# Kernel tuning notes

Measured on AMD Instinct MI355X. Metric: run time of the kernel, lower is better.

The kernel has to match this reference:

```python
import jax, jax.numpy as jnp
import numpy as np

EPS = 1e-8
TEMPERATURE = 1.0


def setup_inputs() -> dict:
    key = jax.random.key(0)
    k1, k2, k3 = jax.random.split(key, 3)
    B, Q, K, H, D = 64, 64, 8192, 1, 64
    return {
        "query": jax.random.normal(k1, (B, Q, H, D), dtype=jnp.float32),
        "key": jax.random.normal(k2, (B, K, H, D), dtype=jnp.float32),
        "value": jax.random.normal(k3, (B, K, H, D), dtype=jnp.float32),
    }


def reference(query, key, value):
    # InvertedDotProductAttention(norm_type='mean', multi_head=False)
    d = query.shape[-1]
    q = query / jnp.sqrt(jnp.asarray(d, query.dtype))
    # logits: [B, H, Q, K]
    attn = jnp.einsum("bqhd,bkhd->bhqk", q, key)
    # inverted attention: softmax over the QUERY axis (-2)
    attn = jax.nn.softmax(attn / TEMPERATURE, axis=-2)
    attn = jnp.clip(attn, 0.0, 1.0)
    # renormalize over keys (norm_type == 'mean')
    attn = attn / (jnp.sum(attn, axis=-1, keepdims=True) + EPS)
    out = jnp.einsum("bhqk,bkhd->bqhd", attn, value)
    # single-head: squeeze heads dim
    out = jnp.squeeze(out, axis=-2)          # [B, Q, Dv]
    attn_weights = jnp.squeeze(attn, axis=-3)  # [B, Q, K]
    return out, attn_weights
```

## Files before the change

### kernel.cpp

```cpp
#include <hip/hip_runtime.h>
#include <cstddef>

#define NB 64
#define NQ 64
#define NK 8192
#define ND 64
#define KPB 256
#define KSL 512
#define NSLICE (NK / KSL)

typedef __attribute__((ext_vector_type(8))) short short8_t;
typedef __attribute__((ext_vector_type(8))) unsigned short ushort8_t;
typedef __attribute__((ext_vector_type(4))) unsigned short ushort4_t;
typedef __attribute__((ext_vector_type(4))) float float4_t;

static __device__ __forceinline__ unsigned short f2bf(float f) {
    unsigned b = __float_as_uint(f);
    b += 0x7FFFu + ((b >> 16) & 1u);
    return (unsigned short)(b >> 16);
}
static __device__ __forceinline__ float bf2f(unsigned short u) {
    return __uint_as_float(((unsigned)u) << 16);
}
static __device__ __forceinline__ void split8(const float* f, short8_t& hi, short8_t& lo) {
#pragma unroll
    for (int j = 0; j < 8; ++j) {
        const unsigned u = __float_as_uint(f[j]);
        hi[j] = (short)(u >> 16);
        const float lof = f[j] - __uint_as_float(u & 0xFFFF0000u);
        lo[j] = (short)(__float_as_uint(lof) >> 16);
    }
}

__global__ __launch_bounds__(256, 3) void k_qk_p(
    const float* __restrict__ query,
    const float* __restrict__ key,
    unsigned short* __restrict__ pstore,
    float* __restrict__ rowsum)
{
    __shared__ alignas(16) unsigned short SH[64 * 264];
    unsigned short* Qhi = SH;
    unsigned short* Qlo = SH + 64 * 72;

    const int tid  = threadIdx.x;
    const int b    = blockIdx.y;
    const int k0   = blockIdx.x * KPB;
    const int lane = tid & 63;
    const int w    = tid >> 6;
    const int lq   = lane & 15;
    const int lg   = lane >> 4;

    float kf[16];
    {
        const float* kr = key + ((size_t)b * NK + k0 + w * 64 + lq) * ND + lg * 8;
        *reinterpret_cast<float4*>(kf)      = *reinterpret_cast<const float4*>(kr);
        *reinterpret_cast<float4*>(kf + 4)  = *reinterpret_cast<const float4*>(kr + 4);
        *reinterpret_cast<float4*>(kf + 8)  = *reinterpret_cast<const float4*>(kr + 32);
        *reinterpret_cast<float4*>(kf + 12) = *reinterpret_cast<const float4*>(kr + 36);
    }

    {
        const float* qb = query + (size_t)b * NQ * ND;
#pragma unroll
        for (int i = 0; i < 2; ++i) {
            const int o  = tid + 256 * i;
            const int q  = o >> 3;
            const int d0 = (o & 7) * 8;
            float f[8];
            *reinterpret_cast<float4*>(f)     = *reinterpret_cast<const float4*>(qb + q * ND + d0);
            *reinterpret_cast<float4*>(f + 4) = *reinterpret_cast<const float4*>(qb + q * ND + d0 + 4);
            short8_t h, l8;
            split8(f, h, l8);
            const int n    = q >> 4;
            const int l    = (q & 15) | (((d0 >> 3) & 3) << 4);
            const int dh   = d0 >> 5;
            const int base = l * 72 + n * 16 + dh * 8;
            *reinterpret_cast<short8_t*>(&Qhi[base]) = h;
            *reinterpret_cast<short8_t*>(&Qlo[base]) = l8;
        }
    }
    __syncthreads();

    short8_t bhi[4][2], blo[4][2];
#pragma unroll
    for (int n = 0; n < 4; ++n)
#pragma unroll
        for (int dh = 0; dh < 2; ++dh) {
            const int base = lane * 72 + n * 16 + dh * 8;
            bhi[n][dh] = *reinterpret_cast<const short8_t*>(&Qhi[base]);
            blo[n][dh] = *reinterpret_cast<const short8_t*>(&Qlo[base]);
        }
    __syncthreads();

    unsigned short* pL = SH;
    float rsacc[4] = {0.f, 0.f, 0.f, 0.f};

#pragma unroll 1
    for (int s = 0; s < 4; ++s) {
        const int kbase = k0 + w * 64 + s * 16;

        short8_t ahi[2], alo[2];
        split8(kf, ahi[0], alo[0]);
        split8(kf + 8, ahi[1], alo[1]);

        if (s < 3) {
            const float* kr = key + ((size_t)b * NK + kbase + 16 + lq) * ND + lg * 8;
            *reinterpret_cast<float4*>(kf)      = *reinterpret_cast<const float4*>(kr);
            *reinterpret_cast<float4*>(kf + 4)  = *reinterpret_cast<const float4*>(kr + 4);
            *reinterpret_cast<float4*>(kf + 8)  = *reinterpret_cast<const float4*>(kr + 32);
            *reinterpret_cast<float4*>(kf + 12) = *reinterpret_cast<const float4*>(kr + 36);
        }

        float4_t acc[4];
#pragma unroll
        for (int n = 0; n < 4; ++n) acc[n] = (float4_t){0.f, 0.f, 0.f, 0.f};
#pragma unroll
        for (int n = 0; n < 4; ++n)
#pragma unroll
            for (int dh = 0; dh < 2; ++dh) {
                acc[n] = __builtin_amdgcn_mfma_f32_16x16x32_bf16(ahi[dh], bhi[n][dh], acc[n], 0, 0, 0);
                acc[n] = __builtin_amdgcn_mfma_f32_16x16x32_bf16(ahi[dh], blo[n][dh], acc[n], 0, 0, 0);
                acc[n] = __builtin_amdgcn_mfma_f32_16x16x32_bf16(alo[dh], bhi[n][dh], acc[n], 0, 0, 0);
            }

        float m[4], z[4];
#pragma unroll
        for (int r = 0; r < 4; ++r) {
            m[r] = fmaxf(fmaxf(acc[0][r], acc[1][r]), fmaxf(acc[2][r], acc[3][r]));
            m[r] = fmaxf(m[r], __shfl_xor(m[r], 1, 64));
            m[r] = fmaxf(m[r], __shfl_xor(m[r], 2, 64));
            m[r] = fmaxf(m[r], __shfl_xor(m[r], 4, 64));
            m[r] = fmaxf(m[r], __shfl_xor(m[r], 8, 64));
            z[r] = 0.f;
        }
#pragma unroll
        for (int n = 0; n < 4; ++n)
#pragma unroll
            for (int r = 0; r < 4; ++r) {
                acc[n][r] = __expf((acc[n][r] - m[r]) * 0.125f);
                z[r] += acc[n][r];
            }
#pragma unroll
        for (int r = 0; r < 4; ++r) {
            z[r] += __shfl_xor(z[r], 1, 64);
            z[r] += __shfl_xor(z[r], 2, 64);
            z[r] += __shfl_xor(z[r], 4, 64);
            z[r] += __shfl_xor(z[r], 8, 64);
            z[r] = 1.f / z[r];
        }

#pragma unroll
        for (int n = 0; n < 4; ++n) {
            ushort4_t u;
            float rs = 0.f;
#pragma unroll
            for (int r = 0; r < 4; ++r) {
                u[r] = f2bf(acc[n][r] * z[r]);
                rs += bf2f(u[r]);
            }
            *reinterpret_cast<ushort4_t*>(
                &pL[(16 * n + lq) * 264 + w * 64 + s * 16 + lg * 4]) = u;
            rs += __shfl_xor(rs, 16, 64);
            rs += __shfl_xor(rs, 32, 64);
            rsacc[n] += rs;
        }
    }

    if (lg == 0) {
#pragma unroll
        for (int n = 0; n < 4; ++n)
            atomicAdd(&rowsum[b * NQ + lq + 16 * n], rsacc[n]);
    }
    __syncthreads();

    {
        const int cl = tid & 63;
#pragma unroll
        for (int t = 0; t < 16; ++t) {
            const int row = t * 4 + w;
            const ushort4_t u = *reinterpret_cast<const ushort4_t*>(&pL[row * 264 + cl * 4]);
            const int c      = cl * 4;
            const int half   = c >> 7;
            const int slot   = (c & 127) >> 3;
            const int sub    = (c >> 2) & 1;
            const int sp     = slot ^ (row & 7);
            *reinterpret_cast<ushort4_t*>(pstore +
                ((size_t)(b * NQ + row)) * NK + k0 + half * 128 + sp * 8 + sub * 4) = u;
        }
    }
}

template<bool PART>
__global__ __launch_bounds__(256, 4) void k_scale_pv(
    const unsigned short* __restrict__ psrc,
    const float* __restrict__ value,
    const float* __restrict__ rowsum,
    float* __restrict__ attn,
    float* __restrict__ dst)
{
    __shared__ alignas(16) unsigned short pLu[64 * 128];
    __shared__ float rsL[NQ];

    const int tid  = threadIdx.x;
    const int b    = blockIdx.y;
    const int ks   = blockIdx.x;
    const int k0   = ks * KSL;
    const int lane = tid & 63;
    const int w    = tid >> 6;
    const int lq   = lane & 15;
    const int lg   = lane >> 4;

    if (tid < NQ) rsL[tid] = 1.f / (rowsum[b * NQ + tid] + 1e-8f);

    const unsigned short* pg = psrc + (size_t)b * NQ * NK;
    const float* vcol = value + ((size_t)b * NK + k0) * ND + 16 * w + lq;

    ushort8_t rp[4];
    float vfA[32], vfB[32];

#define LOADP(HT)                                                              \
    {                                                                          \
        _Pragma("unroll")                                                      \
        for (int i = 0; i < 4; ++i) {                                          \
            const int idx = tid + 256 * i;                                     \
            rp[i] = *reinterpret_cast<const ushort8_t*>(                       \
                &pg[(size_t)(idx >> 4) * NK + k0 + (HT) * 128 + (idx & 15) * 8]); \
        }                                                                      \
    }

#define LOADV(VF, HT)                                                          \
    {                                                                          \
        _Pragma("unroll")                                                      \
        for (int h = 0; h < 4; ++h) {                                          \
            _Pragma("unroll")                                                  \
            for (int j = 0; j < 8; ++j)                                        \
                VF[h * 8 + j] =                                                \
                    vcol[(size_t)((HT) * 128 + h * 32 + lg * 8 + j) * ND];     \
        }                                                                      \
    }

#define STAGE_P(HT)                                                            \
    {                                                                          \
        _Pragma("unroll")                                                      \
        for (int i = 0; i < 4; ++i) {                                          \
            const int idx  = tid + 256 * i;                                    \
            const int row  = idx >> 4;                                         \
            const int sl   = idx & 15;                                         \
            const int slog = sl ^ (row & 7);                                   \
            const float iv = rsL[row];                                         \
            float f[8];                                                        \
            ushort8_t u;                                                       \
            _Pragma("unroll")                                                  \
            for (int j = 0; j < 8; ++j) {                                      \
                f[j] = bf2f(rp[i][j]) * iv;                                    \
                u[j] = f2bf(f[j]);                                             \
            }                                                                  \
            float* ap = attn + ((size_t)(b * NQ + row)) * NK + k0 +            \
                        (HT) * 128 + slog * 8;                                 \
            *reinterpret_cast<float4*>(ap)     = *reinterpret_cast<float4*>(f);     \
            *reinterpret_cast<float4*>(ap + 4) = *reinterpret_cast<float4*>(f + 4); \
            *reinterpret_cast<ushort8_t*>(&pLu[idx * 8]) = u;                  \
        }                                                                      \
    }

#define PVSTEP(VF)                                                             \
    {                                                                          \
        _Pragma("unroll")                                                      \
        for (int h = 0; h < 4; ++h) {                                          \
            short8_t vb;                                                       \
            _Pragma("unroll")                                                  \
            for (int j = 0; j < 8; ++j) vb[j] = (short)f2bf(VF[h * 8 + j]);    \
            _Pragma("unroll")                                                  \
            for (int n = 0; n < 4; ++n) {                                      \
                const short8_t pa = *reinterpret_cast<const short8_t*>(        \
                    &pLu[(16 * n + lq) * 128 + (((h * 4 + lg) ^ (lq & 7)) * 8)]); \
                oacc[n] = __builtin_amdgcn_mfma_f32_16x16x32_bf16(pa, vb, oacc[n], 0, 0, 0); \
            }                                                                  \
        }                                                                      \
    }

    float4_t oacc[4];
#pragma unroll
    for (int n = 0; n < 4; ++n) oacc[n] = (float4_t){0.f, 0.f, 0.f, 0.f};

    LOADP(0); LOADV(vfA, 0);

    __syncthreads();
    STAGE_P(0);
    LOADP(1); LOADV(vfB, 1);
    __syncthreads();
    PVSTEP(vfA);
    __syncthreads();
    STAGE_P(1);
    LOADP(2); LOADV(vfA, 2);
    __syncthreads();
    PVSTEP(vfB);
    __syncthreads();
    STAGE_P(2);
    LOADP(3); LOADV(vfB, 3);
    __syncthreads();
    PVSTEP(vfA);
    __syncthreads();
    STAGE_P(3);
    __syncthreads();
    PVSTEP(vfB);

#undef LOADP
#undef LOADV
#undef STAGE_P
#undef PVSTEP

    if (PART) {
        float* pb = dst + ((size_t)(b * NSLICE + ks)) * (NQ * ND);
#pragma unroll
        for (int n = 0; n < 4; ++n)
#pragma unroll
            for (int r = 0; r < 4; ++r)
                pb[(16 * n + 4 * lg + r) * ND + 16 * w + lq] = oacc[n][r];
    } else {
#pragma unroll
        for (int n = 0; n < 4; ++n)
#pragma unroll
            for (int r = 0; r < 4; ++r)
                atomicAdd(dst + ((size_t)(b * NQ + 16 * n + 4 * lg + r)) * ND + 16 * w + lq,
                          oacc[n][r]);
    }
}

__global__ __launch_bounds__(256) void k_reduce_out(
    const float* __restrict__ partials,
    float* __restrict__ out)
{
    const int b   = blockIdx.y;
    const int idx = blockIdx.x * 256 + threadIdx.x;
    const float4* pb = reinterpret_cast<const float4*>(partials + (size_t)b * NSLICE * NQ * ND);
    float4 sum = make_float4(0.f, 0.f, 0.f, 0.f);
#pragma unroll
    for (int s = 0; s < NSLICE; ++s) {
        const float4 v = pb[(size_t)s * (NQ * ND / 4) + idx];
        sum.x += v.x; sum.y += v.y; sum.z += v.z; sum.w += v.w;
    }
    reinterpret_cast<float4*>(out + (size_t)b * NQ * ND)[idx] = sum;
}

extern "C" void kernel_launch(void* const* d_in, const int* in_sizes, int n_in,
                              void* d_out, int out_size, void* d_ws, size_t ws_size,
                              hipStream_t stream) {
    const float* query = (const float*)d_in[0];
    const float* key   = (const float*)d_in[1];
    const float* value = (const float*)d_in[2];

    float* out  = (float*)d_out;
    float* attn = (float*)d_out + (size_t)NB * NQ * ND;

    const size_t PB_BYTES   = (size_t)NB * NQ * NK * sizeof(unsigned short);
    const size_t PART_BYTES = (size_t)NB * NSLICE * NQ * ND * sizeof(float);

    float* rowsum = (float*)d_ws;
    unsigned short* pbuf = (unsigned short*)((char*)d_ws + 16384);
    float* partials = (float*)((char*)d_ws + 16384 + PB_BYTES);
    const bool part = ws_size >= 16384 + PB_BYTES + PART_BYTES;

    hipMemsetAsync(rowsum, 0, (size_t)NB * NQ * sizeof(float), stream);
    if (!part)
        hipMemsetAsync(out, 0, (size_t)NB * NQ * ND * sizeof(float), stream);

    dim3 gA(NK / KPB, NB);
    k_qk_p<<<gA, 256, 0, stream>>>(query, key, pbuf, rowsum);

    dim3 gB(NK / KSL, NB);
    if (part) {
        k_scale_pv<true><<<gB, 256, 0, stream>>>(pbuf, value, rowsum, attn, partials);
        k_reduce_out<<<dim3(4, NB), 256, 0, stream>>>(partials, out);
    } else {
        k_scale_pv<false><<<gB, 256, 0, stream>>>(pbuf, value, rowsum, attn, out);
    }
}
```

Before: 122.5 us.

## Fuse PV product into QK kernel and defer row normalization to output

Moves the P·V matmul into the QK/softmax kernel, using unnormalized P from shared memory and loading V per 256-key tile. The final row-sum normalization is applied afterwards, in the reduction or a separate scaling kernel. The attention-weight scaling becomes a standalone streaming kernel that reads bf16 P and writes fp32 attn. This removes a sync-heavy staging pipeline, at the cost of more registers in the fused kernel and a partial-sum buffer twice as large.

```diff
diff --git a/kernel.cpp b/kernel.cpp
--- a/kernel.cpp
+++ b/kernel.cpp
@@ -6,8 +6,7 @@
 #define NK 8192
 #define ND 64
 #define KPB 256
-#define KSL 512
-#define NSLICE (NK / KSL)
+#define NSLICE (NK / KPB)
 
 typedef __attribute__((ext_vector_type(8))) short short8_t;
 typedef __attribute__((ext_vector_type(8))) unsigned short ushort8_t;
@@ -32,11 +31,14 @@
     }
 }
 
-__global__ __launch_bounds__(256, 3) void k_qk_p(
+template<bool PART>
+__global__ __launch_bounds__(256, 3) void k_fused(
     const float* __restrict__ query,
     const float* __restrict__ key,
+    const float* __restrict__ value,
     unsigned short* __restrict__ pstore,
-    float* __restrict__ rowsum)
+    float* __restrict__ rowsum,
+    float* __restrict__ dst)
 {
     __shared__ alignas(16) unsigned short SH[64 * 264];
     unsigned short* Qhi = SH;
@@ -49,6 +51,19 @@
     const int w    = tid >> 6;
     const int lq   = lane & 15;
     const int lg   = lane >> 4;
+
+    const float* vcol = value + ((size_t)b * NK + k0) * ND + 16 * w + lq;
+    float vfA[16], vfB[16];
+#pragma unroll
+    for (int h = 0; h < 2; ++h)
+#pragma unroll
+        for (int j = 0; j < 8; ++j)
+            vfA[h * 8 + j] = vcol[(size_t)(h * 32 + lg * 8 + j) * ND];
+#pragma unroll
+    for (int h = 0; h < 2; ++h)
+#pragma unroll
+        for (int j = 0; j < 8; ++j)
+            vfB[h * 8 + j] = vcol[(size_t)(64 + h * 32 + lg * 8 + j) * ND];
 
     float kf[16];
     {
@@ -159,7 +174,7 @@
                 rs += bf2f(u[r]);
             }
             *reinterpret_cast<ushort4_t*>(
-                &pL[(16 * n + lq) * 264 + w * 64 + s * 16 + lg * 4]) = u;
+                &pL[(16 * n + lq) * 264 + (kbase - k0) + lg * 4]) = u;
             rs += __shfl_xor(rs, 16, 64);
             rs += __shfl_xor(rs, 32, 64);
             rsacc[n] += rs;
@@ -173,145 +188,45 @@
     }
     __syncthreads();
 
-    {
-        const int cl = tid & 63;
-#pragma unroll
-        for (int t = 0; t < 16; ++t) {
-            const int row = t * 4 + w;
-            const ushort4_t u = *reinterpret_cast<const ushort4_t*>(&pL[row * 264 + cl * 4]);
-            const int c      = cl * 4;
-            const int half   = c >> 7;
-            const int slot   = (c & 127) >> 3;
-            const int sub    = (c >> 2) & 1;
-            const int sp     = slot ^ (row & 7);
-            *reinterpret_cast<ushort4_t*>(pstore +
-                ((size_t)(b * NQ + row)) * NK + k0 + half * 128 + sp * 8 + sub * 4) = u;
-        }
-    }
-}
-
-template<bool PART>
-__global__ __launch_bounds__(256, 4) void k_scale_pv(
-    const unsigned short* __restrict__ psrc,
-    const float* __restrict__ value,
-    const float* __restrict__ rowsum,
-    float* __restrict__ attn,
-    float* __restrict__ dst)
-{
-    __shared__ alignas(16) unsigned short pLu[64 * 128];
-    __shared__ float rsL[NQ];
-
-    const int tid  = threadIdx.x;
-    const int b    = blockIdx.y;
-    const int ks   = blockIdx.x;
-    const int k0   = ks * KSL;
-    const int lane = tid & 63;
-    const int w    = tid >> 6;
-    const int lq   = lane & 15;
-    const int lg   = lane >> 4;
-
-    if (tid < NQ) rsL[tid] = 1.f / (rowsum[b * NQ + tid] + 1e-8f);
-
-    const unsigned short* pg = psrc + (size_t)b * NQ * NK;
-    const float* vcol = value + ((size_t)b * NK + k0) * ND + 16 * w + lq;
-
-    ushort8_t rp[4];
-    float vfA[32], vfB[32];
-
-#define LOADP(HT)                                                              \
+    float4_t oacc[4];
+#pragma unroll
+    for (int n = 0; n < 4; ++n) oacc[n] = (float4_t){0.f, 0.f, 0.f, 0.f};
+
+#define PVCHUNK(VF, C)                                                         \
     {                                                                          \
         _Pragma("unroll")                                                      \
-        for (int i = 0; i < 4; ++i) {                                          \
-            const int idx = tid + 256 * i;                                     \
-            rp[i] = *reinterpret_cast<const ushort8_t*>(                       \
-                &pg[(size_t)(idx >> 4) * NK + k0 + (HT) * 128 + (idx & 15) * 8]); \
-        }                                                                      \
-    }
-
-#define LOADV(VF, HT)                                                          \
-    {                                                                          \
-        _Pragma("unroll")                                                      \
-        for (int h = 0; h < 4; ++h) {                                          \
-            _Pragma("unroll")                                                  \
-            for (int j = 0; j < 8; ++j)                                        \
-                VF[h * 8 + j] =                                                \
-                    vcol[(size_t)((HT) * 128 + h * 32 + lg * 8 + j) * ND];     \
-        }                                                                      \
-    }
-
-#define STAGE_P(HT)                                                            \
-    {                                                                          \
-        _Pragma("unroll")                                                      \
-        for (int i = 0; i < 4; ++i) {                                          \
-            const int idx  = tid + 256 * i;                                    \
-            const int row  = idx >> 4;                                         \
-            const int sl   = idx & 15;                                         \
-            const int slog = sl ^ (row & 7);                                   \
-            const float iv = rsL[row];                                         \
-            float f[8];                                                        \
-            ushort8_t u;                                                       \
-            _Pragma("unroll")                                                  \
-            for (int j = 0; j < 8; ++j) {                                      \
-                f[j] = bf2f(rp[i][j]) * iv;                                    \
-                u[j] = f2bf(f[j]);                                             \
-            }                                                                  \
-            float* ap = attn + ((size_t)(b * NQ + row)) * NK + k0 +            \
-                        (HT) * 128 + slog * 8;                                 \
-            *reinterpret_cast<float4*>(ap)     = *reinterpret_cast<float4*>(f);     \
-            *reinterpret_cast<float4*>(ap + 4) = *reinterpret_cast<float4*>(f + 4); \
-            *reinterpret_cast<ushort8_t*>(&pLu[idx * 8]) = u;                  \
-        }                                                                      \
-    }
-
-#define PVSTEP(VF)                                                             \
-    {                                                                          \
-        _Pragma("unroll")                                                      \
-        for (int h = 0; h < 4; ++h) {                                          \
+        for (int h = 0; h < 2; ++h) {                                          \
             short8_t vb;                                                       \
             _Pragma("unroll")                                                  \
             for (int j = 0; j < 8; ++j) vb[j] = (short)f2bf(VF[h * 8 + j]);    \
             _Pragma("unroll")                                                  \
             for (int n = 0; n < 4; ++n) {                                      \
                 const short8_t pa = *reinterpret_cast<const short8_t*>(        \
-                    &pLu[(16 * n + lq) * 128 + (((h * 4 + lg) ^ (lq & 7)) * 8)]); \
+                    &pL[(16 * n + lq) * 264 + (C) * 64 + h * 32 + lg * 8]);    \
                 oacc[n] = __builtin_amdgcn_mfma_f32_16x16x32_bf16(pa, vb, oacc[n], 0, 0, 0); \
             }                                                                  \
         }                                                                      \
     }
-
-    float4_t oacc[4];
-#pragma unroll
-    for (int n = 0; n < 4; ++n) oacc[n] = (float4_t){0.f, 0.f, 0.f, 0.f};
-
-    LOADP(0); LOADV(vfA, 0);
-
-    __syncthreads();
-    STAGE_P(0);
-    LOADP(1); LOADV(vfB, 1);
-    __syncthreads();
-    PVSTEP(vfA);
-    __syncthreads();
-    STAGE_P(1);
-    LOADP(2); LOADV(vfA, 2);
-    __syncthreads();
-    PVSTEP(vfB);
-    __syncthreads();
-    STAGE_P(2);
-    LOADP(3); LOADV(vfB, 3);
-    __syncthreads();
-    PVSTEP(vfA);
-    __syncthreads();
-    STAGE_P(3);
-    __syncthreads();
-    PVSTEP(vfB);
-
-#undef LOADP
-#undef LOADV
-#undef STAGE_P
-#undef PVSTEP
+#define LOADVF(VF, C)                                                          \
+    {                                                                          \
+        _Pragma("unroll")                                                      \
+        for (int h = 0; h < 2; ++h)                                            \
+            _Pragma("unroll")                                                  \
+            for (int j = 0; j < 8; ++j)                                        \
+                VF[h * 8 + j] = vcol[(size_t)((C) * 64 + h * 32 + lg * 8 + j) * ND]; \
+    }
+
+    PVCHUNK(vfA, 0);
+    LOADVF(vfA, 2);
+    PVCHUNK(vfB, 1);
+    LOADVF(vfB, 3);
+    PVCHUNK(vfA, 2);
+    PVCHUNK(vfB, 3);
+#undef PVCHUNK
+#undef LOADVF
 
     if (PART) {
-        float* pb = dst + ((size_t)(b * NSLICE + ks)) * (NQ * ND);
+        float* pb = dst + ((size_t)(b * NSLICE + blockIdx.x)) * (NQ * ND);
 #pragma unroll
         for (int n = 0; n < 4; ++n)
 #pragma unroll
@@ -325,14 +240,53 @@
                 atomicAdd(dst + ((size_t)(b * NQ + 16 * n + 4 * lg + r)) * ND + 16 * w + lq,
                           oacc[n][r]);
     }
+
+    {
+        const int cl = tid & 63;
+#pragma unroll
+        for (int t = 0; t < 16; ++t) {
+            const int row = t * 4 + w;
+            const ushort4_t u = *reinterpret_cast<const ushort4_t*>(&pL[row * 264 + cl * 4]);
+            *reinterpret_cast<ushort4_t*>(pstore +
+                ((size_t)(b * NQ + row)) * NK + k0 + cl * 4) = u;
+        }
+    }
+}
+
+__global__ __launch_bounds__(256) void k_scale(
+    const unsigned short* __restrict__ psrc,
+    const float* __restrict__ rowsum,
+    float* __restrict__ attn)
+{
+    const int b   = blockIdx.y;
+    const int row = blockIdx.x * 4 + (threadIdx.x >> 6);
+    const int cl  = threadIdx.x & 63;
+
+    const float iv = 1.f / (rowsum[b * NQ + row] + 1e-8f);
+    const unsigned short* pr = psrc + ((size_t)(b * NQ + row)) * NK;
+    float* ar = attn + ((size_t)(b * NQ + row)) * NK;
+
+#pragma unroll
+    for (int it = 0; it < 16; ++it) {
+        const int i8 = it * 64 + cl;
+        const ushort8_t u = *reinterpret_cast<const ushort8_t*>(&pr[i8 * 8]);
+        float f[8];
+#pragma unroll
+        for (int j = 0; j < 8; ++j) f[j] = bf2f(u[j]) * iv;
+        *reinterpret_cast<float4*>(&ar[i8 * 8])     = *reinterpret_cast<float4*>(f);
+        *reinterpret_cast<float4*>(&ar[i8 * 8 + 4]) = *reinterpret_cast<float4*>(f + 4);
+    }
 }
 
 __global__ __launch_bounds__(256) void k_reduce_out(
     const float* __restrict__ partials,
+    const float* __restrict__ rowsum,
     float* __restrict__ out)
 {
     const int b   = blockIdx.y;
     const int idx = blockIdx.x * 256 + threadIdx.x;
+    const int q   = idx >> 4;
+    const float iv = 1.f / (rowsum[b * NQ + q] + 1e-8f);
     const float4* pb = reinterpret_cast<const float4*>(partials + (size_t)b * NSLICE * NQ * ND);
     float4 sum = make_float4(0.f, 0.f, 0.f, 0.f);
 #pragma unroll
@@ -340,7 +294,22 @@
         const float4 v = pb[(size_t)s * (NQ * ND / 4) + idx];
         sum.x += v.x; sum.y += v.y; sum.z += v.z; sum.w += v.w;
     }
+    sum.x *= iv; sum.y *= iv; sum.z *= iv; sum.w *= iv;
     reinterpret_cast<float4*>(out + (size_t)b * NQ * ND)[idx] = sum;
+}
+
+__global__ __launch_bounds__(256) void k_norm_out(
+    const float* __restrict__ rowsum,
+    float* __restrict__ out)
+{
+    const int b   = blockIdx.y;
+    const int idx = blockIdx.x * 256 + threadIdx.x;
+    const int q   = idx >> 4;
+    const float iv = 1.f / (rowsum[b * NQ + q] + 1e-8f);
+    float4* op = reinterpret_cast<float4*>(out + (size_t)b * NQ * ND) + idx;
+    float4 v = *op;
+    v.x *= iv; v.y *= iv; v.z *= iv; v.w *= iv;
+    *op = v;
 }
 
 extern "C" void kernel_launch(void* const* d_in, const int* in_sizes, int n_in,
@@ -365,14 +334,14 @@
     if (!part)
         hipMemsetAsync(out, 0, (size_t)NB * NQ * ND * sizeof(float), stream);
 
-    dim3 gA(NK / KPB, NB);
-    k_qk_p<<<gA, 256, 0, stream>>>(query, key, pbuf, rowsum);
-
-    dim3 gB(NK / KSL, NB);
+    dim3 g(NK / KPB, NB);
     if (part) {
-        k_scale_pv<true><<<gB, 256, 0, stream>>>(pbuf, value, rowsum, attn, partials);
-        k_reduce_out<<<dim3(4, NB), 256, 0, stream>>>(partials, out);
+        k_fused<true><<<g, 256, 0, stream>>>(query, key, value, pbuf, rowsum, partials);
+        k_scale<<<dim3(NQ / 4, NB), 256, 0, stream>>>(pbuf, rowsum, attn);
+        k_reduce_out<<<dim3(4, NB), 256, 0, stream>>>(partials, rowsum, out);
     } else {
-        k_scale_pv<false><<<gB, 256, 0, stream>>>(pbuf, value, rowsum, attn, out);
-    }
-}
+        k_fused<false><<<g, 256, 0, stream>>>(query, key, value, pbuf, rowsum, out);
+        k_scale<<<dim3(NQ / 4, NB), 256, 0, stream>>>(pbuf, rowsum, attn);
+        k_norm_out<<<dim3(4, NB), 256, 0, stream>>>(rowsum, out);
+    }
+}
```

After: 130.7 us. 1.07x slower.
